# Optimization experiments

Hardware: AMD Instinct MI355X
Metric: run time of the kernel (lower is better)

The kernel has to match this reference:

```python
import jax, jax.numpy as jnp
import numpy as np

D_MODEL = 256
NUM_HEADS = 4
HEAD_DIM = D_MODEL // NUM_HEADS


def setup_inputs() -> dict:
    key = jax.random.key(0)
    ks = jax.random.split(key, 16)
    B, N, M, C = 2, 256, 256, D_MODEL
    inp = {
        'q_tokens': jax.random.normal(ks[0], (B, N, C), jnp.float32),
        'k_tokens': jax.random.normal(ks[1], (B, M, C), jnp.float32),
        'v_tokens': jax.random.normal(ks[2], (B, M, C), jnp.float32),
        'qk_embeds': jax.random.normal(ks[3], (B, N, M, C), jnp.float32),
        'qv_embeds': jax.random.normal(ks[4], (B, N, M, C), jnp.float32),
    }
    scale = 1.0 / np.sqrt(C)
    # Linear layer params (weight used as x @ W + b)
    inp['Wq'] = jax.random.normal(ks[5], (C, C), jnp.float32) * scale
    inp['bq'] = jnp.zeros((C,), jnp.float32)
    inp['Wk'] = jax.random.normal(ks[6], (C, C), jnp.float32) * scale
    inp['bk'] = jnp.zeros((C,), jnp.float32)
    inp['Wv'] = jax.random.normal(ks[7], (C, C), jnp.float32) * scale
    inp['bv'] = jnp.zeros((C,), jnp.float32)
    inp['Wqk'] = jax.random.normal(ks[8], (C, C), jnp.float32) * scale
    inp['bqk'] = jnp.zeros((C,), jnp.float32)
    inp['Wqv'] = jax.random.normal(ks[9], (C, C), jnp.float32) * scale
    inp['bqv'] = jnp.zeros((C,), jnp.float32)
    return inp


def reference(q_tokens, k_tokens, v_tokens, qk_embeds, qv_embeds,
              Wq, bq, Wk, bk, Wv, bv, Wqk, bqk, Wqv, bqv):
    B, N, C = q_tokens.shape
    M = k_tokens.shape[1]
    H, hc = NUM_HEADS, HEAD_DIM

    # token projections -> (B, H, len, hc)
    q = (q_tokens @ Wq + bq).reshape(B, N, H, hc).transpose(0, 2, 1, 3)
    k = (k_tokens @ Wk + bk).reshape(B, M, H, hc).transpose(0, 2, 1, 3)
    v = (v_tokens @ Wv + bv).reshape(B, M, H, hc).transpose(0, 2, 1, 3)

    # pair-embedding projections -> (B, N, M, H, hc)
    qk = (qk_embeds @ Wqk + bqk).reshape(B, N, M, H, hc)
    qv = (qv_embeds @ Wqv + bqv).reshape(B, N, M, H, hc)

    # scores: q . (k + qk)  == q.k + q.qk
    scores = jnp.einsum('bhnc,bhmc->bhnm', q, k)
    scores = scores + jnp.einsum('bhnc,bnmhc->bhnm', q, qk)
    scores = scores / np.sqrt(hc).astype(np.float32)

    attn = jax.nn.softmax(scores, axis=-1)  # (B, H, N, M)

    # output: attn @ (v + qv) == attn@v + attn.qv
    hidden = jnp.einsum('bhnm,bhmc->bhnc', attn, v)
    hidden = hidden + jnp.einsum('bhnm,bnmhc->bhnc', attn, qv)
    hidden = hidden.transpose(0, 2, 1, 3).reshape(B, N, C)  # (B, N, C)
    return hidden, attn
```

## Files before the change

### kernel.cpp

```cpp
#include <hip/hip_runtime.h>

#define BB 2
#define NN 256
#define CC 256

__device__ __forceinline__ float dot4acc(float4 e, float4 w, float s) {
    s = fmaf(e.x, w.x, s); s = fmaf(e.y, w.y, s);
    s = fmaf(e.z, w.z, s); s = fmaf(e.w, w.w, s);
    return s;
}

__global__ __launch_bounds__(256) void proj_gemm(
    const float* __restrict__ q_tok, const float* __restrict__ k_tok, const float* __restrict__ v_tok,
    const float* __restrict__ Wq, const float* __restrict__ bq,
    const float* __restrict__ Wk, const float* __restrict__ bk,
    const float* __restrict__ Wv, const float* __restrict__ bv,
    float* __restrict__ out)
{
    const int row0 = blockIdx.x * 64;
    const int col0 = blockIdx.y * 64;
    const int seg  = row0 >> 9;
    const float* A    = seg == 0 ? q_tok : (seg == 1 ? k_tok : v_tok);
    const float* W    = seg == 0 ? Wq    : (seg == 1 ? Wk    : Wv);
    const float* bias = seg == 0 ? bq    : (seg == 1 ? bk    : bv);
    const int ar0 = row0 & 511;

    __shared__ float As[64][17];
    __shared__ float Bs[16][68];
    const int t  = threadIdx.x;
    const int tr = t >> 4, tc = t & 15;
    float acc[4][4] = {};

    const int sr  = t >> 2, sk4 = (t & 3) << 2;
    const int bkr = t >> 4, bj4 = (t & 15) << 2;

    for (int k0 = 0; k0 < 256; k0 += 16) {
        float4 a4 = *reinterpret_cast<const float4*>(&A[(ar0 + sr) * 256 + k0 + sk4]);
        float4 b4 = *reinterpret_cast<const float4*>(&W[(k0 + bkr) * 256 + col0 + bj4]);
        As[sr][sk4 + 0] = a4.x; As[sr][sk4 + 1] = a4.y; As[sr][sk4 + 2] = a4.z; As[sr][sk4 + 3] = a4.w;
        Bs[bkr][bj4 + 0] = b4.x; Bs[bkr][bj4 + 1] = b4.y; Bs[bkr][bj4 + 2] = b4.z; Bs[bkr][bj4 + 3] = b4.w;
        __syncthreads();
        #pragma unroll
        for (int k = 0; k < 16; ++k) {
            float a[4], bbv[4];
            #pragma unroll
            for (int i = 0; i < 4; ++i) a[i] = As[tr * 4 + i][k];
            #pragma unroll
            for (int j = 0; j < 4; ++j) bbv[j] = Bs[k][tc * 4 + j];
            #pragma unroll
            for (int i = 0; i < 4; ++i)
                #pragma unroll
                for (int j = 0; j < 4; ++j)
                    acc[i][j] = fmaf(a[i], bbv[j], acc[i][j]);
        }
        __syncthreads();
    }
    #pragma unroll
    for (int i = 0; i < 4; ++i) {
        const int r = row0 + tr * 4 + i;
        #pragma unroll
        for (int j = 0; j < 4; ++j) {
            const int cj = col0 + tc * 4 + j;
            out[r * 256 + cj] = acc[i][j] + bias[cj];
        }
    }
}

__global__ __launch_bounds__(256) void qw_gemm(
    const float* __restrict__ qp, const float* __restrict__ Wqk, float* __restrict__ qW)
{
    const int h    = blockIdx.z;
    const int row0 = blockIdx.x * 64;
    const int d0   = blockIdx.y * 64;
    __shared__ float As[64][17];
    __shared__ float Bs[16][68];
    const int t  = threadIdx.x;
    const int tr = t >> 4, tc = t & 15;
    float acc[4][4] = {};
    const int sr = t >> 2, sc4 = (t & 3) << 2;

    for (int k0 = 0; k0 < 64; k0 += 16) {
        float4 a4 = *reinterpret_cast<const float4*>(&qp[(row0 + sr) * 256 + h * 64 + k0 + sc4]);
        float4 b4 = *reinterpret_cast<const float4*>(&Wqk[(d0 + sr) * 256 + h * 64 + k0 + sc4]);
        As[sr][sc4 + 0] = a4.x; As[sr][sc4 + 1] = a4.y; As[sr][sc4 + 2] = a4.z; As[sr][sc4 + 3] = a4.w;
        Bs[sc4 + 0][sr] = b4.x; Bs[sc4 + 1][sr] = b4.y; Bs[sc4 + 2][sr] = b4.z; Bs[sc4 + 3][sr] = b4.w;
        __syncthreads();
        #pragma unroll
        for (int k = 0; k < 16; ++k) {
            float a[4], bbv[4];
            #pragma unroll
            for (int i = 0; i < 4; ++i) a[i] = As[tr * 4 + i][k];
            #pragma unroll
            for (int j = 0; j < 4; ++j) bbv[j] = Bs[k][tc * 4 + j];
            #pragma unroll
            for (int i = 0; i < 4; ++i)
                #pragma unroll
                for (int j = 0; j < 4; ++j)
                    acc[i][j] = fmaf(a[i], bbv[j], acc[i][j]);
        }
        __syncthreads();
    }
    #pragma unroll
    for (int i = 0; i < 4; ++i)
        #pragma unroll
        for (int j = 0; j < 4; ++j)
            qW[((row0 + tr * 4 + i) * 4 + h) * 256 + d0 + tc * 4 + j] = acc[i][j];
}

__global__ __launch_bounds__(256) void qk_gemm(
    const float* __restrict__ qkvp, float* __restrict__ Sqk)
{
    const int bh = blockIdx.z;
    const int b  = bh >> 2, h = bh & 3;
    const int n0 = blockIdx.x * 64;
    const int m0 = blockIdx.y * 64;
    __shared__ float As[64][17];
    __shared__ float Bs[16][68];
    const int t  = threadIdx.x;
    const int tr = t >> 4, tc = t & 15;
    float acc[4][4] = {};
    const int sr = t >> 2, sc4 = (t & 3) << 2;

    for (int k0 = 0; k0 < 64; k0 += 16) {
        float4 a4 = *reinterpret_cast<const float4*>(&qkvp[(size_t)(b * 256 + n0 + sr) * 256 + h * 64 + k0 + sc4]);
        float4 b4 = *reinterpret_cast<const float4*>(&qkvp[(size_t)(512 + b * 256 + m0 + sr) * 256 + h * 64 + k0 + sc4]);
        As[sr][sc4 + 0] = a4.x; As[sr][sc4 + 1] = a4.y; As[sr][sc4 + 2] = a4.z; As[sr][sc4 + 3] = a4.w;
        Bs[sc4 + 0][sr] = b4.x; Bs[sc4 + 1][sr] = b4.y; Bs[sc4 + 2][sr] = b4.z; Bs[sc4 + 3][sr] = b4.w;
        __syncthreads();
        #pragma unroll
        for (int k = 0; k < 16; ++k) {
            float a[4], bbv[4];
            #pragma unroll
            for (int i = 0; i < 4; ++i) a[i] = As[tr * 4 + i][k];
            #pragma unroll
            for (int j = 0; j < 4; ++j) bbv[j] = Bs[k][tc * 4 + j];
            #pragma unroll
            for (int i = 0; i < 4; ++i)
                #pragma unroll
                for (int j = 0; j < 4; ++j)
                    acc[i][j] = fmaf(a[i], bbv[j], acc[i][j]);
        }
        __syncthreads();
    }
    #pragma unroll
    for (int i = 0; i < 4; ++i)
        #pragma unroll
        for (int j = 0; j < 4; ++j)
            Sqk[(size_t)((b * 4 + h) * 256 + n0 + tr * 4 + i) * 256 + m0 + tc * 4 + j] = acc[i][j];
}

__global__ __launch_bounds__(512, 4) void mega2(
    const float* __restrict__ qk_emb, const float* __restrict__ qv_emb,
    const float* __restrict__ qkvp, const float* __restrict__ qW,
    const float* __restrict__ Sqk, const float* __restrict__ Wqv,
    const float* __restrict__ bqv,
    float* __restrict__ attn_out, float* __restrict__ hidden)
{
    const int bn = blockIdx.x;
    const int b  = bn >> 8, n = bn & 255;
    const int t  = threadIdx.x;
    const int w  = t >> 6, l = t & 63;

    __shared__ float U[4096];
    float* qWs = U;
    float* Ssc = U + 1024;
    float* Ap  = U;
    __shared__ float attn_s[4][256];
    __shared__ float stage[16][256];
    __shared__ float pr[2][256];
    __shared__ float red[16];

    if (t < 256)
        *reinterpret_cast<float4*>(&U[t * 4]) =
            *reinterpret_cast<const float4*>(&qW[(size_t)bn * 1024 + t * 4]);
    __syncthreads();

    {
        const int lq = l & 15, lr = l >> 4;
        #pragma unroll
        for (int g = 0; g < 8; g += 2) {
            const int m0 = w * 32 + g * 4 + lr;
            const float* r0 = qk_emb + (size_t)(bn * 256 + m0) * 256 + lq * 4;
            const float* r1 = r0 + 1024;
            const float4 e00 = *reinterpret_cast<const float4*>(r0);
            const float4 e01 = *reinterpret_cast<const float4*>(r0 + 64);
            const float4 e02 = *reinterpret_cast<const float4*>(r0 + 128);
            const float4 e03 = *reinterpret_cast<const float4*>(r0 + 192);
            const float4 e10 = *reinterpret_cast<const float4*>(r1);
            const float4 e11 = *reinterpret_cast<const float4*>(r1 + 64);
            const float4 e12 = *reinterpret_cast<const float4*>(r1 + 128);
            const float4 e13 = *reinterpret_cast<const float4*>(r1 + 192);
            float p0[4], p1[4];
            #pragma unroll
            for (int hh = 0; hh < 4; ++hh) {
                const float4 w0 = *reinterpret_cast<const float4*>(&qWs[hh * 256 + lq * 4]);
                const float4 w1 = *reinterpret_cast<const float4*>(&qWs[hh * 256 + 64 + lq * 4]);
                const float4 w2 = *reinterpret_cast<const float4*>(&qWs[hh * 256 + 128 + lq * 4]);
                const float4 w3 = *reinterpret_cast<const float4*>(&qWs[hh * 256 + 192 + lq * 4]);
                float s0 = 0.f, s1 = 0.f;
                s0 = dot4acc(e00, w0, s0); s0 = dot4acc(e01, w1, s0);
                s0 = dot4acc(e02, w2, s0); s0 = dot4acc(e03, w3, s0);
                s1 = dot4acc(e10, w0, s1); s1 = dot4acc(e11, w1, s1);
                s1 = dot4acc(e12, w2, s1); s1 = dot4acc(e13, w3, s1);
                p0[hh] = s0; p1[hh] = s1;
            }
            #pragma unroll
            for (int hh = 0; hh < 4; ++hh) {
                p0[hh] += __shfl_xor(p0[hh], 1); p1[hh] += __shfl_xor(p1[hh], 1);
                p0[hh] += __shfl_xor(p0[hh], 2); p1[hh] += __shfl_xor(p1[hh], 2);
                p0[hh] += __shfl_xor(p0[hh], 4); p1[hh] += __shfl_xor(p1[hh], 4);
                p0[hh] += __shfl_xor(p0[hh], 8); p1[hh] += __shfl_xor(p1[hh], 8);
            }
            if (lq == 0) {
                #pragma unroll
                for (int hh = 0; hh < 4; ++hh) {
                    Ssc[hh * 256 + m0]     = p0[hh];
                    Ssc[hh * 256 + m0 + 4] = p1[hh];
                }
            }
        }
    }
    __syncthreads();

    {
        const int h = t >> 7, j = t & 127;
        const size_t srow = (size_t)((b * 4 + h) * 256 + n) * 256;
        const float sv0 = (Ssc[h * 256 + j]       + Sqk[srow + j])       * 0.125f;
        const float sv1 = (Ssc[h * 256 + j + 128] + Sqk[srow + j + 128]) * 0.125f;

        float mx = fmaxf(sv0, sv1);
        #pragma unroll
        for (int mask = 32; mask >= 1; mask >>= 1) mx = fmaxf(mx, __shfl_xor(mx, mask));
        if (l == 0) red[w] = mx;
        __syncthreads();
        mx = fmaxf(red[h * 2], red[h * 2 + 1]);
        const float e0 = __expf(sv0 - mx), e1 = __expf(sv1 - mx);
        float sum = e0 + e1;
        #pragma unroll
        for (int mask = 32; mask >= 1; mask >>= 1) sum += __shfl_xor(sum, mask);
        if (l == 0) red[8 + w] = sum;
        __syncthreads();
        const float inv = 1.f / (red[8 + h * 2] + red[8 + h * 2 + 1]);
        const float a0 = e0 * inv, a1 = e1 * inv;
        attn_s[h][j]       = a0;
        attn_s[h][j + 128] = a1;
        float* ao = attn_out + (size_t)((b * 4 + h) * 256 + n) * 256;
        ao[j]       = a0;
        ao[j + 128] = a1;
    }
    __syncthreads();

    {
        float4 acc[4];
        #pragma unroll
        for (int hh = 0; hh < 4; ++hh) acc[hh] = make_float4(0.f, 0.f, 0.f, 0.f);
        const float* rb = qv_emb + (size_t)(bn * 256 + w * 32) * 256 + l * 4;
        #pragma unroll
        for (int mm = 0; mm < 32; mm += 8) {
            float4 e[8];
            #pragma unroll
            for (int r = 0; r < 8; ++r)
                e[r] = *reinterpret_cast<const float4*>(rb + (size_t)(mm + r) * 256);
            #pragma unroll
            for (int r = 0; r < 8; ++r) {
                #pragma unroll
                for (int hh = 0; hh < 4; ++hh) {
                    const float a = attn_s[hh][w * 32 + mm + r];
                    acc[hh].x = fmaf(a, e[r].x, acc[hh].x);
                    acc[hh].y = fmaf(a, e[r].y, acc[hh].y);
                    acc[hh].z = fmaf(a, e[r].z, acc[hh].z);
                    acc[hh].w = fmaf(a, e[r].w, acc[hh].w);
                }
            }
        }
        if (w < 4) {
            #pragma unroll
            for (int hh = 0; hh < 4; ++hh)
                *reinterpret_cast<float4*>(&Ap[(w * 4 + hh) * 256 + l * 4]) = acc[hh];
        }
        __syncthreads();
        if (w >= 4) {
            #pragma unroll
            for (int hh = 0; hh < 4; ++hh) {
                float4* p = reinterpret_cast<float4*>(&Ap[((w - 4) * 4 + hh) * 256 + l * 4]);
                float4 o = *p;
                o.x += acc[hh].x; o.y += acc[hh].y; o.z += acc[hh].z; o.w += acc[hh].w;
                *p = o;
            }
        }
        __syncthreads();
        #pragma unroll
        for (int i = 0; i < 2; ++i) {
            const int idx = t + i * 512;
            const int hh = idx >> 8, d = idx & 255;
            Ap[hh * 256 + d] = Ap[hh * 256 + d] + Ap[(4 + hh) * 256 + d]
                             + Ap[(8 + hh) * 256 + d] + Ap[(12 + hh) * 256 + d];
        }
    }
    __syncthreads();

    {
        const int c = t & 255, half = t >> 8, hc = c >> 6;
        float hv = 0.f;
        for (int mt = 0; mt < 16; ++mt) {
            #pragma unroll
            for (int i = 0; i < 2; ++i) {
                const int fidx = t + i * 512;
                const int row = fidx >> 6, col4 = (fidx & 63) * 4;
                *reinterpret_cast<float4*>(&stage[row][col4]) =
                    *reinterpret_cast<const float4*>(
                        &qkvp[(size_t)(1024 + b * 256 + mt * 16 + row) * 256 + col4]);
            }
            __syncthreads();
            #pragma unroll
            for (int r = 0; r < 8; ++r)
                hv = fmaf(attn_s[hc][mt * 16 + half * 8 + r], stage[half * 8 + r][c], hv);
            __syncthreads();
        }
        for (int dt = 0; dt < 16; ++dt) {
            #pragma unroll
            for (int i = 0; i < 2; ++i) {
                const int fidx = t + i * 512;
                const int row = fidx >> 6, col4 = (fidx & 63) * 4;
                *reinterpret_cast<float4*>(&stage[row][col4]) =
                    *reinterpret_cast<const float4*>(&Wqv[(size_t)(dt * 16 + row) * 256 + col4]);
            }
            __syncthreads();
            #pragma unroll
            for (int r = 0; r < 8; ++r)
                hv = fmaf(U[hc * 256 + dt * 16 + half * 8 + r], stage[half * 8 + r][c], hv);
            __syncthreads();
        }
        pr[half][c] = hv;
    }
    __syncthreads();
    if (t < 256)
        hidden[(size_t)bn * 256 + t] = pr[0][t] + pr[1][t] + bqv[t];
}

extern "C" void kernel_launch(void* const* d_in, const int* in_sizes, int n_in,
                              void* d_out, int out_size, void* d_ws, size_t ws_size,
                              hipStream_t stream) {
    (void)in_sizes; (void)n_in; (void)out_size; (void)ws_size;
    const float* q_tok  = (const float*)d_in[0];
    const float* k_tok  = (const float*)d_in[1];
    const float* v_tok  = (const float*)d_in[2];
    const float* qk_emb = (const float*)d_in[3];
    const float* qv_emb = (const float*)d_in[4];
    const float* Wq  = (const float*)d_in[5];   const float* bq  = (const float*)d_in[6];
    const float* Wk  = (const float*)d_in[7];   const float* bk  = (const float*)d_in[8];
    const float* Wv  = (const float*)d_in[9];   const float* bv  = (const float*)d_in[10];
    const float* Wqk = (const float*)d_in[11];
    const float* Wqv = (const float*)d_in[13];  const float* bqv = (const float*)d_in[14];

    float* ws   = (float*)d_ws;
    float* qkvp = ws;
    float* qW   = ws + 393216;
    float* Sqk  = ws + 917504;

    float* hidden = (float*)d_out;
    float* attn   = (float*)d_out + BB * NN * CC;

    proj_gemm<<<dim3(24, 4),   256, 0, stream>>>(q_tok, k_tok, v_tok, Wq, bq, Wk, bk, Wv, bv, qkvp);
    qw_gemm  <<<dim3(8, 4, 4), 256, 0, stream>>>(qkvp, Wqk, qW);
    qk_gemm  <<<dim3(4, 4, 8), 256, 0, stream>>>(qkvp, Sqk);
    mega2    <<<512,           512, 0, stream>>>(qk_emb, qv_emb, qkvp, qW, Sqk, Wqv, bqv, attn, hidden);
}
```

Measured before the change: 93.62 us.

## Use per-warp online softmax to overlap qv_emb streaming with score computation

Each warp now computes a local max and sum over its own 32 keys and immediately accumulates attn-weighted qv_emb with unnormalized weights. The per-warp partials are rescaled once after a single cross-warp merge, which removes the block-wide barriers between the score, softmax and qv phases. Sqk is preloaded into shared memory, and the V/Wqv staging loop now register-prefetches the next tile so global loads overlap compute. Shared-memory use grows because buffers no longer alias, which may reduce occupancy.

```diff
diff --git a/kernel.cpp b/kernel.cpp
--- a/kernel.cpp
+++ b/kernel.cpp
@@ -149,7 +149,7 @@
             Sqk[(size_t)((b * 4 + h) * 256 + n0 + tr * 4 + i) * 256 + m0 + tc * 4 + j] = acc[i][j];
 }
 
-__global__ __launch_bounds__(512, 4) void mega2(
+__global__ __launch_bounds__(512, 4) void mega3(
     const float* __restrict__ qk_emb, const float* __restrict__ qv_emb,
     const float* __restrict__ qkvp, const float* __restrict__ qW,
     const float* __restrict__ Sqk, const float* __restrict__ Wqv,
@@ -161,99 +161,95 @@
     const int t  = threadIdx.x;
     const int w  = t >> 6, l = t & 63;
 
-    __shared__ float U[4096];
-    float* qWs = U;
-    float* Ssc = U + 1024;
-    float* Ap  = U;
-    __shared__ float attn_s[4][256];
+    __shared__ float qWs[1024];
+    __shared__ float SqkL[1024];
+    __shared__ float Ssc[1024];
+    __shared__ float attn_s[1024];
+    __shared__ float Ap[4096];
     __shared__ float stage[16][256];
     __shared__ float pr[2][256];
-    __shared__ float red[16];
+    __shared__ float mxs[8][4], sums[8][4], scl[8][4];
 
     if (t < 256)
-        *reinterpret_cast<float4*>(&U[t * 4]) =
+        *reinterpret_cast<float4*>(&qWs[t * 4]) =
             *reinterpret_cast<const float4*>(&qW[(size_t)bn * 1024 + t * 4]);
     __syncthreads();
 
+    const int lq = l & 15, lr = l >> 4, li = l & 31;
+
+    if (l < 32) {
+        #pragma unroll
+        for (int h = 0; h < 4; ++h)
+            SqkL[h * 256 + w * 32 + li] =
+                Sqk[(size_t)((b * 4 + h) * 256 + n) * 256 + w * 32 + li];
+    }
+
+    #pragma unroll
+    for (int g = 0; g < 8; g += 2) {
+        const int m0 = w * 32 + g * 4 + lr;
+        const float* r0 = qk_emb + (size_t)(bn * 256 + m0) * 256 + lq * 4;
+        const float* r1 = r0 + 1024;
+        const float4 e00 = *reinterpret_cast<const float4*>(r0);
+        const float4 e01 = *reinterpret_cast<const float4*>(r0 + 64);
+        const float4 e02 = *reinterpret_cast<const float4*>(r0 + 128);
+        const float4 e03 = *reinterpret_cast<const float4*>(r0 + 192);
+        const float4 e10 = *reinterpret_cast<const float4*>(r1);
+        const float4 e11 = *reinterpret_cast<const float4*>(r1 + 64);
+        const float4 e12 = *reinterpret_cast<const float4*>(r1 + 128);
+        const float4 e13 = *reinterpret_cast<const float4*>(r1 + 192);
+        float p0[4], p1[4];
+        #pragma unroll
+        for (int hh = 0; hh < 4; ++hh) {
+            const float4 w0 = *reinterpret_cast<const float4*>(&qWs[hh * 256 + lq * 4]);
+            const float4 w1 = *reinterpret_cast<const float4*>(&qWs[hh * 256 + 64 + lq * 4]);
+            const float4 w2 = *reinterpret_cast<const float4*>(&qWs[hh * 256 + 128 + lq * 4]);
+            const float4 w3 = *reinterpret_cast<const float4*>(&qWs[hh * 256 + 192 + lq * 4]);
+            float s0 = 0.f, s1 = 0.f;
+            s0 = dot4acc(e00, w0, s0); s0 = dot4acc(e01, w1, s0);
+            s0 = dot4acc(e02, w2, s0); s0 = dot4acc(e03, w3, s0);
+            s1 = dot4acc(e10, w0, s1); s1 = dot4acc(e11, w1, s1);
+            s1 = dot4acc(e12, w2, s1); s1 = dot4acc(e13, w3, s1);
+            p0[hh] = s0; p1[hh] = s1;
+        }
+        #pragma unroll
+        for (int hh = 0; hh < 4; ++hh) {
+            p0[hh] += __shfl_xor(p0[hh], 1); p1[hh] += __shfl_xor(p1[hh], 1);
+            p0[hh] += __shfl_xor(p0[hh], 2); p1[hh] += __shfl_xor(p1[hh], 2);
+            p0[hh] += __shfl_xor(p0[hh], 4); p1[hh] += __shfl_xor(p1[hh], 4);
+            p0[hh] += __shfl_xor(p0[hh], 8); p1[hh] += __shfl_xor(p1[hh], 8);
+        }
+        if (lq == 0) {
+            #pragma unroll
+            for (int hh = 0; hh < 4; ++hh) {
+                Ssc[hh * 256 + m0]     = p0[hh];
+                Ssc[hh * 256 + m0 + 4] = p1[hh];
+            }
+        }
+    }
+
+    float mxw[4], smw[4];
+    #pragma unroll
+    for (int h = 0; h < 4; ++h) {
+        const float sc = (Ssc[h * 256 + w * 32 + li] + SqkL[h * 256 + w * 32 + li]) * 0.125f;
+        float mx = sc;
+        #pragma unroll
+        for (int mask = 16; mask >= 1; mask >>= 1) mx = fmaxf(mx, __shfl_xor(mx, mask));
+        const float e = __expf(sc - mx);
+        attn_s[h * 256 + w * 32 + li] = e;
+        float sm = e;
+        #pragma unroll
+        for (int mask = 16; mask >= 1; mask >>= 1) sm += __shfl_xor(sm, mask);
+        mxw[h] = mx; smw[h] = sm;
+    }
+    if (l == 0) {
+        #pragma unroll
+        for (int h = 0; h < 4; ++h) { mxs[w][h] = mxw[h]; sums[w][h] = smw[h]; }
+    }
+
+    float4 acc[4];
+    #pragma unroll
+    for (int hh = 0; hh < 4; ++hh) acc[hh] = make_float4(0.f, 0.f, 0.f, 0.f);
     {
-        const int lq = l & 15, lr = l >> 4;
-        #pragma unroll
-        for (int g = 0; g < 8; g += 2) {
-            const int m0 = w * 32 + g * 4 + lr;
-            const float* r0 = qk_emb + (size_t)(bn * 256 + m0) * 256 + lq * 4;
-            const float* r1 = r0 + 1024;
-            const float4 e00 = *reinterpret_cast<const float4*>(r0);
-            const float4 e01 = *reinterpret_cast<const float4*>(r0 + 64);
-            const float4 e02 = *reinterpret_cast<const float4*>(r0 + 128);
-            const float4 e03 = *reinterpret_cast<const float4*>(r0 + 192);
-            const float4 e10 = *reinterpret_cast<const float4*>(r1);
-            const float4 e11 = *reinterpret_cast<const float4*>(r1 + 64);
-            const float4 e12 = *reinterpret_cast<const float4*>(r1 + 128);
-            const float4 e13 = *reinterpret_cast<const float4*>(r1 + 192);
-            float p0[4], p1[4];
-            #pragma unroll
-            for (int hh = 0; hh < 4; ++hh) {
-                const float4 w0 = *reinterpret_cast<const float4*>(&qWs[hh * 256 + lq * 4]);
-                const float4 w1 = *reinterpret_cast<const float4*>(&qWs[hh * 256 + 64 + lq * 4]);
-                const float4 w2 = *reinterpret_cast<const float4*>(&qWs[hh * 256 + 128 + lq * 4]);
-                const float4 w3 = *reinterpret_cast<const float4*>(&qWs[hh * 256 + 192 + lq * 4]);
-                float s0 = 0.f, s1 = 0.f;
-                s0 = dot4acc(e00, w0, s0); s0 = dot4acc(e01, w1, s0);
-                s0 = dot4acc(e02, w2, s0); s0 = dot4acc(e03, w3, s0);
-                s1 = dot4acc(e10, w0, s1); s1 = dot4acc(e11, w1, s1);
-                s1 = dot4acc(e12, w2, s1); s1 = dot4acc(e13, w3, s1);
-                p0[hh] = s0; p1[hh] = s1;
-            }
-            #pragma unroll
-            for (int hh = 0; hh < 4; ++hh) {
-                p0[hh] += __shfl_xor(p0[hh], 1); p1[hh] += __shfl_xor(p1[hh], 1);
-                p0[hh] += __shfl_xor(p0[hh], 2); p1[hh] += __shfl_xor(p1[hh], 2);
-                p0[hh] += __shfl_xor(p0[hh], 4); p1[hh] += __shfl_xor(p1[hh], 4);
-                p0[hh] += __shfl_xor(p0[hh], 8); p1[hh] += __shfl_xor(p1[hh], 8);
-            }
-            if (lq == 0) {
-                #pragma unroll
-                for (int hh = 0; hh < 4; ++hh) {
-                    Ssc[hh * 256 + m0]     = p0[hh];
-                    Ssc[hh * 256 + m0 + 4] = p1[hh];
-                }
-            }
-        }
-    }
-    __syncthreads();
-
-    {
-        const int h = t >> 7, j = t & 127;
-        const size_t srow = (size_t)((b * 4 + h) * 256 + n) * 256;
-        const float sv0 = (Ssc[h * 256 + j]       + Sqk[srow + j])       * 0.125f;
-        const float sv1 = (Ssc[h * 256 + j + 128] + Sqk[srow + j + 128]) * 0.125f;
-
-        float mx = fmaxf(sv0, sv1);
-        #pragma unroll
-        for (int mask = 32; mask >= 1; mask >>= 1) mx = fmaxf(mx, __shfl_xor(mx, mask));
-        if (l == 0) red[w] = mx;
-        __syncthreads();
-        mx = fmaxf(red[h * 2], red[h * 2 + 1]);
-        const float e0 = __expf(sv0 - mx), e1 = __expf(sv1 - mx);
-        float sum = e0 + e1;
-        #pragma unroll
-        for (int mask = 32; mask >= 1; mask >>= 1) sum += __shfl_xor(sum, mask);
-        if (l == 0) red[8 + w] = sum;
-        __syncthreads();
-        const float inv = 1.f / (red[8 + h * 2] + red[8 + h * 2 + 1]);
-        const float a0 = e0 * inv, a1 = e1 * inv;
-        attn_s[h][j]       = a0;
-        attn_s[h][j + 128] = a1;
-        float* ao = attn_out + (size_t)((b * 4 + h) * 256 + n) * 256;
-        ao[j]       = a0;
-        ao[j + 128] = a1;
-    }
-    __syncthreads();
-
-    {
-        float4 acc[4];
-        #pragma unroll
-        for (int hh = 0; hh < 4; ++hh) acc[hh] = make_float4(0.f, 0.f, 0.f, 0.f);
         const float* rb = qv_emb + (size_t)(bn * 256 + w * 32) * 256 + l * 4;
         #pragma unroll
         for (int mm = 0; mm < 32; mm += 8) {
@@ -265,7 +261,7 @@
             for (int r = 0; r < 8; ++r) {
                 #pragma unroll
                 for (int hh = 0; hh < 4; ++hh) {
-                    const float a = attn_s[hh][w * 32 + mm + r];
+                    const float a = attn_s[hh * 256 + w * 32 + mm + r];
                     acc[hh].x = fmaf(a, e[r].x, acc[hh].x);
                     acc[hh].y = fmaf(a, e[r].y, acc[hh].y);
                     acc[hh].z = fmaf(a, e[r].z, acc[hh].z);
@@ -273,63 +269,100 @@
                 }
             }
         }
-        if (w < 4) {
-            #pragma unroll
-            for (int hh = 0; hh < 4; ++hh)
-                *reinterpret_cast<float4*>(&Ap[(w * 4 + hh) * 256 + l * 4]) = acc[hh];
-        }
-        __syncthreads();
-        if (w >= 4) {
-            #pragma unroll
-            for (int hh = 0; hh < 4; ++hh) {
-                float4* p = reinterpret_cast<float4*>(&Ap[((w - 4) * 4 + hh) * 256 + l * 4]);
-                float4 o = *p;
-                o.x += acc[hh].x; o.y += acc[hh].y; o.z += acc[hh].z; o.w += acc[hh].w;
-                *p = o;
-            }
-        }
-        __syncthreads();
-        #pragma unroll
-        for (int i = 0; i < 2; ++i) {
-            const int idx = t + i * 512;
-            const int hh = idx >> 8, d = idx & 255;
-            Ap[hh * 256 + d] = Ap[hh * 256 + d] + Ap[(4 + hh) * 256 + d]
-                             + Ap[(8 + hh) * 256 + d] + Ap[(12 + hh) * 256 + d];
-        }
-    }
-    __syncthreads();
+    }
+    __syncthreads();
+
+    if (t < 4) {
+        const int h = t;
+        float mg = mxs[0][h];
+        #pragma unroll
+        for (int ww = 1; ww < 8; ++ww) mg = fmaxf(mg, mxs[ww][h]);
+        float sr[8]; float sg = 0.f;
+        #pragma unroll
+        for (int ww = 0; ww < 8; ++ww) { sr[ww] = __expf(mxs[ww][h] - mg); sg += sums[ww][h] * sr[ww]; }
+        const float inv = 1.f / sg;
+        #pragma unroll
+        for (int ww = 0; ww < 8; ++ww) scl[ww][h] = sr[ww] * inv;
+    }
+    __syncthreads();
+
+    {
+        const int h = t >> 7, j = t & 127;
+        float* ao = attn_out + (size_t)((b * 4 + h) * 256 + n) * 256;
+        #pragma unroll
+        for (int rep = 0; rep < 2; ++rep) {
+            const int jj = j + rep * 128;
+            const float a = attn_s[h * 256 + jj] * scl[jj >> 5][h];
+            attn_s[h * 256 + jj] = a;
+            ao[jj] = a;
+        }
+    }
+    if (w < 4) {
+        #pragma unroll
+        for (int hh = 0; hh < 4; ++hh) {
+            const float s = scl[w][hh];
+            float4 v = acc[hh];
+            v.x *= s; v.y *= s; v.z *= s; v.w *= s;
+            *reinterpret_cast<float4*>(&Ap[(w * 4 + hh) * 256 + l * 4]) = v;
+        }
+    }
+    __syncthreads();
+    if (w >= 4) {
+        #pragma unroll
+        for (int hh = 0; hh < 4; ++hh) {
+            const float s = scl[w][hh];
+            float4* p = reinterpret_cast<float4*>(&Ap[((w - 4) * 4 + hh) * 256 + l * 4]);
+            float4 o = *p;
+            o.x = fmaf(acc[hh].x, s, o.x); o.y = fmaf(acc[hh].y, s, o.y);
+            o.z = fmaf(acc[hh].z, s, o.z); o.w = fmaf(acc[hh].w, s, o.w);
+            *p = o;
+        }
+    }
+    __syncthreads();
+    #pragma unroll
+    for (int i = 0; i < 2; ++i) {
+        const int idx = t + i * 512;
+        const int hh = idx >> 8, d = idx & 255;
+        Ap[hh * 256 + d] = Ap[hh * 256 + d] + Ap[(4 + hh) * 256 + d]
+                         + Ap[(8 + hh) * 256 + d] + Ap[(12 + hh) * 256 + d];
+    }
 
     {
         const int c = t & 255, half = t >> 8, hc = c >> 6;
+        const int fr0 = t >> 6, fc0 = (t & 63) * 4;
+        const int fr1 = fr0 + 8;
+        const float* vbase = qkvp + (size_t)(1024 + b * 256) * 256;
+        float4 ra = *reinterpret_cast<const float4*>(&vbase[(size_t)fr0 * 256 + fc0]);
+        float4 rb = *reinterpret_cast<const float4*>(&vbase[(size_t)fr1 * 256 + fc0]);
         float hv = 0.f;
         for (int mt = 0; mt < 16; ++mt) {
-            #pragma unroll
-            for (int i = 0; i < 2; ++i) {
-                const int fidx = t + i * 512;
-                const int row = fidx >> 6, col4 = (fidx & 63) * 4;
-                *reinterpret_cast<float4*>(&stage[row][col4]) =
-                    *reinterpret_cast<const float4*>(
-                        &qkvp[(size_t)(1024 + b * 256 + mt * 16 + row) * 256 + col4]);
+            __syncthreads();
+            *reinterpret_cast<float4*>(&stage[fr0][fc0]) = ra;
+            *reinterpret_cast<float4*>(&stage[fr1][fc0]) = rb;
+            if (mt < 15) {
+                ra = *reinterpret_cast<const float4*>(&vbase[(size_t)((mt + 1) * 16 + fr0) * 256 + fc0]);
+                rb = *reinterpret_cast<const float4*>(&vbase[(size_t)((mt + 1) * 16 + fr1) * 256 + fc0]);
+            } else {
+                ra = *reinterpret_cast<const float4*>(&Wqv[(size_t)fr0 * 256 + fc0]);
+                rb = *reinterpret_cast<const float4*>(&Wqv[(size_t)fr1 * 256 + fc0]);
             }
             __syncthreads();
             #pragma unroll
             for (int r = 0; r < 8; ++r)
-                hv = fmaf(attn_s[hc][mt * 16 + half * 8 + r], stage[half * 8 + r][c], hv);
+                hv = fmaf(attn_s[hc * 256 + mt * 16 + half * 8 + r], stage[half * 8 + r][c], hv);
+        }
+        for (int dt = 0; dt < 16; ++dt) {
             __syncthreads();
-        }
-        for (int dt = 0; dt < 16; ++dt) {
-            #pragma unroll
-            for (int i = 0; i < 2; ++i) {
-                const int fidx = t + i * 512;
-                const int row = fidx >> 6, col4 = (fidx & 63) * 4;
-                *reinterpret_cast<float4*>(&stage[row][col4]) =
-                    *reinterpret_cast<const float4*>(&Wqv[(size_t)(dt * 16 + row) * 256 + col4]);
+            *reinterpret_cast<float4*>(&stage[fr0][fc0]) = ra;
+            *reinterpret_cast<float4*>(&stage[fr1][fc0]) = rb;
+            if (dt < 15) {
+                ra = *reinterpret_cast<const float4*>(&Wqv[(size_t)((dt + 1) * 16 + fr0) * 256 + fc0]);
+                rb = *reinterpret_cast<const float4*>(&Wqv[(size_t)((dt + 1) * 16 + fr1) * 256 + fc0]);
             }
             __syncthreads();
             #pragma unroll
             for (int r = 0; r < 8; ++r)
-                hv = fmaf(U[hc * 256 + dt * 16 + half * 8 + r], stage[half * 8 + r][c], hv);
-            __syncthreads();
+                hv = fmaf(Ap[hc * 256 + dt * 16 + half * 8 + r], stage[half * 8 + r][c], hv);
         }
         pr[half][c] = hv;
     }
@@ -364,5 +397,5 @@
     proj_gemm<<<dim3(24, 4),   256, 0, stream>>>(q_tok, k_tok, v_tok, Wq, bq, Wk, bk, Wv, bv, qkvp);
     qw_gemm  <<<dim3(8, 4, 4), 256, 0, stream>>>(qkvp, Wqk, qW);
     qk_gemm  <<<dim3(4, 4, 8), 256, 0, stream>>>(qkvp, Sqk);
-    mega2    <<<512,           512, 0, stream>>>(qk_emb, qv_emb, qkvp, qW, Sqk, Wqv, bqv, attn, hidden);
-}
+    mega3    <<<512,           512, 0, stream>>>(qk_emb, qv_emb, qkvp, qW, Sqk, Wqv, bqv, attn, hidden);
+}
```

Result: no change. 92.13 us (-1.6%).
